# Kernel optimization log

Hardware: AMD Instinct MI355X
Metric: run time of the kernel (lower is better)

Reference implementation:

```python
import jax, jax.numpy as jnp
import numpy as np

N = 50000          # nodes
E = 1_600_000      # directed edges (before self loops)
G = 128            # graphs in batch
IN_F = 64
C1, H = 32, 4      # gat1: out_channels=32, heads=4 -> hidden 128
C2 = 64            # gat2: out_channels=64, heads=1, concat=False
OUT_F = 2
EPS = 1e-5
NEG_SLOPE = 0.2    # PyG GATv2Conv default


def setup_inputs() -> dict:
    key = jax.random.key(0)
    ks = jax.random.split(key, 24)
    s = 0.05
    inp = {
        'x': jax.random.normal(ks[0], (N, IN_F), jnp.float32),
        'edge_index': jax.random.randint(ks[1], (2, E), 0, N, dtype=jnp.int64),
        'batch': jnp.sort(jax.random.randint(ks[2], (N,), 0, G, dtype=jnp.int64)),
        # GATv2 layer 1 (in=64 -> 4 heads x 32)
        'W1l': jax.random.normal(ks[3], (IN_F, H * C1), jnp.float32) * s,
        'b1l': jnp.zeros((H * C1,), jnp.float32),
        'W1r': jax.random.normal(ks[4], (IN_F, H * C1), jnp.float32) * s,
        'b1r': jnp.zeros((H * C1,), jnp.float32),
        'att1': jax.random.normal(ks[5], (H, C1), jnp.float32) * s,
        'bias1': jnp.zeros((H * C1,), jnp.float32),
        # GATv2 layer 2 (in=128 -> 1 head x 64, no concat)
        'W2l': jax.random.normal(ks[6], (H * C1, C2), jnp.float32) * s,
        'b2l': jnp.zeros((C2,), jnp.float32),
        'W2r': jax.random.normal(ks[7], (H * C1, C2), jnp.float32) * s,
        'b2r': jnp.zeros((C2,), jnp.float32),
        'att2': jax.random.normal(ks[8], (1, C2), jnp.float32) * s,
        'bias2': jnp.zeros((C2,), jnp.float32),
        # batchnorms (batch-statistics normalization)
        'bn1_g': jnp.ones((H * C1,), jnp.float32),
        'bn1_b': jnp.zeros((H * C1,), jnp.float32),
        'bn2_g': jnp.ones((C2,), jnp.float32),
        'bn2_b': jnp.zeros((C2,), jnp.float32),
        # final linear: CL2_F*3 -> out_f
        'lin_w': jax.random.normal(ks[9], (3 * C2, OUT_F), jnp.float32) * s,
        'lin_b': jnp.zeros((OUT_F,), jnp.float32),
    }
    return inp


def _gatv2(x, Wl, bl, Wr, br, att, bias, src, dst, heads, ch, concat, n_nodes):
    # x: [N, F_in]; src/dst: [E'] (self loops already appended)
    xl = (x @ Wl + bl).reshape(n_nodes, heads, ch)  # source transform
    xr = (x @ Wr + br).reshape(n_nodes, heads, ch)  # target transform
    m = jax.nn.leaky_relu(xl[src] + xr[dst], NEG_SLOPE)      # [E', H, C]
    logits = jnp.einsum('ehc,hc->eh', m, att)                # [E', H]
    # segment softmax over destination nodes (every node has a self loop)
    mx = jax.ops.segment_max(logits, dst, num_segments=n_nodes)
    a = jnp.exp(logits - mx[dst])
    denom = jax.ops.segment_sum(a, dst, num_segments=n_nodes)
    alpha = a / denom[dst]                                   # [E', H]
    out = jax.ops.segment_sum(xl[src] * alpha[..., None], dst,
                              num_segments=n_nodes)          # [N, H, C]
    if concat:
        out = out.reshape(n_nodes, heads * ch)
    else:
        out = out.mean(axis=1)
    return out + bias


def _bn(h, gamma, beta):
    mu = h.mean(axis=0)
    var = h.var(axis=0)
    return (h - mu) * jax.lax.rsqrt(var + EPS) * gamma + beta


def reference(x, edge_index, batch, W1l, b1l, W1r, b1r, att1, bias1,
              W2l, b2l, W2r, b2r, att2, bias2,
              bn1_g, bn1_b, bn2_g, bn2_b, lin_w, lin_b):
    n = x.shape[0]
    loops = jnp.arange(n, dtype=edge_index.dtype)
    src = jnp.concatenate([edge_index[0], loops])  # PyG add_self_loops=True
    dst = jnp.concatenate([edge_index[1], loops])

    h = jax.nn.relu(_gatv2(x, W1l, b1l, W1r, b1r, att1, bias1,
                           src, dst, H, C1, True, n))
    h = _bn(h, bn1_g, bn1_b)      # dropout is identity (eval)
    h = jax.nn.relu(_gatv2(h, W2l, b2l, W2r, b2r, att2, bias2,
                           src, dst, 1, C2, False, n))
    h = _bn(h, bn2_g, bn2_b)

    x0 = jax.ops.segment_sum(h, batch, num_segments=G)                  # add pool
    cnt = jax.ops.segment_sum(jnp.ones((n, 1), h.dtype), batch, num_segments=G)
    x1 = x0 / jnp.maximum(cnt, 1.0)                                     # mean pool
    x2 = jax.ops.segment_max(h, batch, num_segments=G)                  # max pool
    feat = jnp.concatenate([x0, x1, x2], axis=-1)                       # [G, 3*C2]
    return feat @ lin_w + lin_b
```

## Files before the change

kernel.cpp:

```cpp
#include <hip/hip_runtime.h>
#include <hip/hip_fp16.h>
#include <math.h>

#define BSHIFT 7
#define CHUNK  8192
#define CAP    6144

__device__ inline __half2 habs2_(__half2 x){
  union { __half2 h; unsigned u; } c; c.h = x; c.u &= 0x7FFF7FFFu; return c.h;
}
__device__ inline __half2 lrelu2_(__half2 x, __half2 c06, __half2 c04){
  return __hfma2(c04, habs2_(x), __hmul2(c06, x));
}

__global__ __launch_bounds__(256) void k_bucket(const int* __restrict__ ei, int E, int N, int NB,
    int* __restrict__ bfill, unsigned* __restrict__ ebuf){
  extern __shared__ int hist[];
  int base = blockIdx.x*CHUNK;
  int EL = E + N;
  int end = min(base + CHUNK, EL);
  for (int i = threadIdx.x; i < NB; i += 256) hist[i] = 0;
  __syncthreads();
  for (int e = base + threadIdx.x; e < end; e += 256){
    int d = (e < E) ? ei[E + e] : (e - E);
    atomicAdd(&hist[d >> BSHIFT], 1);
  }
  __syncthreads();
  for (int b = threadIdx.x; b < NB; b += 256){
    int c = hist[b];
    hist[b] = (c > 0) ? (b*CAP + atomicAdd(&bfill[b], c)) : 0;
  }
  __syncthreads();
  for (int e = base + threadIdx.x; e < end; e += 256){
    int s, d;
    if (e < E){ s = ei[e]; d = ei[E + e]; } else { s = d = e - E; }
    int pos = atomicAdd(&hist[d >> BSHIFT], 1);
    ebuf[pos] = (unsigned)s | ((unsigned)d << 16);
  }
}

__global__ __launch_bounds__(1024) void k_fine(const unsigned* __restrict__ ebuf,
    const int* __restrict__ bfill, int N, int NB,
    int* __restrict__ rstart, int* __restrict__ rend, int* __restrict__ esrc){
  __shared__ int cnt[128];
  __shared__ int sc[128];
  __shared__ int base[128];
  int b = blockIdx.x;
  int n0 = b << BSHIFT;
  int nn = min(128, N - n0);
  int e0 = b*CAP;
  int e1 = e0 + bfill[b];
  if (threadIdx.x < 128) cnt[threadIdx.x] = 0;
  __syncthreads();
  for (int e = e0 + threadIdx.x; e < e1; e += 1024)
    atomicAdd(&cnt[(ebuf[e] >> 16) & 127], 1);
  __syncthreads();
  if (threadIdx.x < 128) sc[threadIdx.x] = cnt[threadIdx.x];
  __syncthreads();
  for (int off = 1; off < 128; off <<= 1){
    int v = 0;
    if (threadIdx.x < 128 && (int)threadIdx.x >= off) v = sc[threadIdx.x - off];
    __syncthreads();
    if (threadIdx.x < 128) sc[threadIdx.x] += v;
    __syncthreads();
  }
  if (threadIdx.x < 128){
    int bs = e0 + sc[threadIdx.x] - cnt[threadIdx.x];
    base[threadIdx.x] = bs;
    if ((int)threadIdx.x < nn){
      rstart[n0 + threadIdx.x] = bs;
      rend[n0 + threadIdx.x]   = bs + cnt[threadIdx.x];
    }
    cnt[threadIdx.x] = 0;
  }
  __syncthreads();
  for (int e = e0 + threadIdx.x; e < e1; e += 1024){
    unsigned pk = ebuf[e];
    int local = (int)(pk >> 16) & 127;
    int pos = base[local] + atomicAdd(&cnt[local], 1);
    esrc[pos] = (int)(pk & 0xffffu);
  }
}

template<int K, int COLS, bool BN, bool INHALF>
__global__ __launch_bounds__(256) void k_gemm(const void* __restrict__ Xv,
    const float* __restrict__ Wl, const float* __restrict__ bl,
    const float* __restrict__ Wr, const float* __restrict__ br,
    __half* __restrict__ outl, __half* __restrict__ outr, int N,
    const float* __restrict__ mu, const float* __restrict__ rstd,
    const float* __restrict__ gam, const float* __restrict__ bet){
  constexpr int HALF = COLS/2;
  constexpr int JG   = COLS/4;
  constexpr int NGRP = 256/JG;
  constexpr int NPG  = 32/NGRP;
  __shared__ float xs[32][K];
  const int tid = threadIdx.x;
  const int n0 = blockIdx.x*32;
  if constexpr (INHALF){
    const __half2* X2 = (const __half2*)Xv;
    for (int t = tid; t < 32*(K/2); t += 256){
      int r = t / (K/2), c2 = t % (K/2), c = c2*2;
      int node = n0 + r;
      float2 v = (node < N) ? __half22float2(X2[(size_t)node*(K/2) + c2]) : make_float2(0.f,0.f);
      if (BN){
        v.x = (v.x - mu[c  ]) * rstd[c  ] * gam[c  ] + bet[c  ];
        v.y = (v.y - mu[c+1]) * rstd[c+1] * gam[c+1] + bet[c+1];
      }
      xs[r][c] = v.x; xs[r][c+1] = v.y;
    }
  } else {
    const float* X = (const float*)Xv;
    for (int t = tid; t < 32*K; t += 256){
      int r = t / K, c = t % K;
      int node = n0 + r;
      xs[r][c] = (node < N) ? X[(size_t)node*K + c] : 0.f;
    }
  }
  __syncthreads();
  const int jg = tid % JG;
  const int ng = tid / JG;
  const int q  = jg*4;
  const bool isL = (q < HALF);
  const float* W = isL ? Wl : Wr;
  const int jj   = isL ? q : q - HALF;
  const float* bb = isL ? bl : br;
  __half* OUT    = isL ? outl : outr;
  const float4 bias4 = *(const float4*)(bb + jj);
  float acc[NPG][4];
  #pragma unroll
  for (int n = 0; n < NPG; ++n){ acc[n][0]=acc[n][1]=acc[n][2]=acc[n][3]=0.f; }
  for (int k = 0; k < K; k += 4){
    const float4 w0 = *(const float4*)(W + (size_t)(k+0)*HALF + jj);
    const float4 w1 = *(const float4*)(W + (size_t)(k+1)*HALF + jj);
    const float4 w2 = *(const float4*)(W + (size_t)(k+2)*HALF + jj);
    const float4 w3 = *(const float4*)(W + (size_t)(k+3)*HALF + jj);
    #pragma unroll
    for (int n = 0; n < NPG; ++n){
      const float4 xv = *(const float4*)(&xs[ng*NPG + n][k]);
      acc[n][0] = fmaf(xv.w,w3.x, fmaf(xv.z,w2.x, fmaf(xv.y,w1.x, fmaf(xv.x,w0.x, acc[n][0]))));
      acc[n][1] = fmaf(xv.w,w3.y, fmaf(xv.z,w2.y, fmaf(xv.y,w1.y, fmaf(xv.x,w0.y, acc[n][1]))));
      acc[n][2] = fmaf(xv.w,w3.z, fmaf(xv.z,w2.z, fmaf(xv.y,w1.z, fmaf(xv.x,w0.z, acc[n][2]))));
      acc[n][3] = fmaf(xv.w,w3.w, fmaf(xv.z,w2.w, fmaf(xv.y,w1.w, fmaf(xv.x,w0.w, acc[n][3]))));
    }
  }
  #pragma unroll
  for (int n = 0; n < NPG; ++n){
    int node = n0 + ng*NPG + n;
    if (node < N){
      union { __half2 h[2]; uint2 u; } cv;
      cv.h[0] = __floats2half2_rn(acc[n][0]+bias4.x, acc[n][1]+bias4.y);
      cv.h[1] = __floats2half2_rn(acc[n][2]+bias4.z, acc[n][3]+bias4.w);
      *(uint2*)(OUT + (size_t)node*HALF + jj) = cv.u;
    }
  }
}

__global__ __launch_bounds__(256) void k_gat1(const __half* __restrict__ xl, const __half* __restrict__ xr,
    const int* __restrict__ rstart, const int* __restrict__ rend,
    const int* __restrict__ esrc,
    const float* __restrict__ att, const float* __restrict__ bias,
    __half* __restrict__ h1, int N){
  int wv = (blockIdx.x*256 + threadIdx.x) >> 6;
  int lane = threadIdx.x & 63;
  int g = lane >> 4;
  int t = lane & 15;
  int node = wv*4 + g;
  bool live = node < N;
  int nd = live ? node : 0;
  int c0 = t*8;
  const __half2 c06 = __float2half2_rn(0.6f);
  const __half2 c04 = __float2half2_rn(0.4f);
  union { uint4 u; __half2 h[4]; } xru;
  xru.u = *(const uint4*)(xr + (size_t)nd*128 + c0);
  float4 a0 = *(const float4*)(att + c0);
  float4 a1 = *(const float4*)(att + c0 + 4);
  __half2 av2[4] = { __floats2half2_rn(a0.x,a0.y), __floats2half2_rn(a0.z,a0.w),
                     __floats2half2_rn(a1.x,a1.y), __floats2half2_rn(a1.z,a1.w) };
  int r0 = live ? rstart[nd] : 0;
  int r1 = live ? rend[nd]   : 0;
  int d  = r1 - r0;
  d = max(d, __shfl_xor(d, 16));
  d = max(d, __shfl_xor(d, 32));
  float s = 0.f;
  __half2 acc2[4];
  #pragma unroll
  for (int k = 0; k < 4; ++k) acc2[k] = __float2half2_rn(0.f);
  #pragma unroll 2
  for (int i = 0; i < d; ++i){
    int e = r0 + i;
    bool valid = e < r1;
    int j = esrc[valid ? e : r0];
    union { uint4 u; __half2 h[4]; } v;
    v.u = *(const uint4*)(xl + (size_t)j*128 + c0);
    __half2 p2 = __float2half2_rn(0.f);
    #pragma unroll
    for (int k = 0; k < 4; ++k){
      __half2 m2 = __hadd2(v.h[k], xru.h[k]);
      p2 = __hfma2(lrelu2_(m2, c06, c04), av2[k], p2);
    }
    float p = __low2float(p2) + __high2float(p2);
    p += __shfl_xor(p, 1);
    p += __shfl_xor(p, 2);
    float w = valid ? __expf(p) : 0.f;
    s += w;
    __half2 w2 = __float2half2_rn(w);
    #pragma unroll
    for (int k = 0; k < 4; ++k) acc2[k] = __hfma2(w2, v.h[k], acc2[k]);
  }
  if (live){
    float inv = 1.f/s;
    float4 b0 = *(const float4*)(bias + c0);
    float4 b1 = *(const float4*)(bias + c0 + 4);
    float bv[8] = {b0.x,b0.y,b0.z,b0.w,b1.x,b1.y,b1.z,b1.w};
    union { __half2 h[4]; uint4 u; } o;
    #pragma unroll
    for (int k = 0; k < 4; ++k){
      float2 af = __half22float2(acc2[k]);
      float f0 = fmaxf(af.x*inv + bv[2*k],   0.f);
      float f1 = fmaxf(af.y*inv + bv[2*k+1], 0.f);
      o.h[k] = __floats2half2_rn(f0, f1);
    }
    *(uint4*)(h1 + (size_t)nd*128 + c0) = o.u;
  }
}

__global__ __launch_bounds__(256) void k_gat2(const __half* __restrict__ xl, const __half* __restrict__ xr,
    const int* __restrict__ rstart, const int* __restrict__ rend,
    const int* __restrict__ esrc,
    const float* __restrict__ att, const float* __restrict__ bias,
    __half* __restrict__ h2, int N){
  int wv = (blockIdx.x*256 + threadIdx.x) >> 6;
  int lane = threadIdx.x & 63;
  int g = lane >> 3;
  int t = lane & 7;
  int node = wv*8 + g;
  bool live = node < N;
  int nd = live ? node : 0;
  int c0 = t*8;
  const __half2 c06 = __float2half2_rn(0.6f);
  const __half2 c04 = __float2half2_rn(0.4f);
  union { uint4 u; __half2 h[4]; } xru;
  xru.u = *(const uint4*)(xr + (size_t)nd*64 + c0);
  float4 a0 = *(const float4*)(att + c0);
  float4 a1 = *(const float4*)(att + c0 + 4);
  __half2 av2[4] = { __floats2half2_rn(a0.x,a0.y), __floats2half2_rn(a0.z,a0.w),
                     __floats2half2_rn(a1.x,a1.y), __floats2half2_rn(a1.z,a1.w) };
  int r0 = live ? rstart[nd] : 0;
  int r1 = live ? rend[nd]   : 0;
  int d  = r1 - r0;
  d = max(d, __shfl_xor(d, 8));
  d = max(d, __shfl_xor(d, 16));
  d = max(d, __shfl_xor(d, 32));
  float s = 0.f;
  __half2 acc2[4];
  #pragma unroll
  for (int k = 0; k < 4; ++k) acc2[k] = __float2half2_rn(0.f);
  #pragma unroll 2
  for (int i = 0; i < d; ++i){
    int e = r0 + i;
    bool valid = e < r1;
    int j = esrc[valid ? e : r0];
    union { uint4 u; __half2 h[4]; } v;
    v.u = *(const uint4*)(xl + (size_t)j*64 + c0);
    __half2 p2 = __float2half2_rn(0.f);
    #pragma unroll
    for (int k = 0; k < 4; ++k){
      __half2 m2 = __hadd2(v.h[k], xru.h[k]);
      p2 = __hfma2(lrelu2_(m2, c06, c04), av2[k], p2);
    }
    float p = __low2float(p2) + __high2float(p2);
    p += __shfl_xor(p, 1);
    p += __shfl_xor(p, 2);
    p += __shfl_xor(p, 4);
    float w = valid ? __expf(p) : 0.f;
    s += w;
    __half2 w2 = __float2half2_rn(w);
    #pragma unroll
    for (int k = 0; k < 4; ++k) acc2[k] = __hfma2(w2, v.h[k], acc2[k]);
  }
  if (live){
    float inv = 1.f/s;
    float4 b0 = *(const float4*)(bias + c0);
    float4 b1 = *(const float4*)(bias + c0 + 4);
    float bv[8] = {b0.x,b0.y,b0.z,b0.w,b1.x,b1.y,b1.z,b1.w};
    union { __half2 h[4]; uint4 u; } o;
    #pragma unroll
    for (int k = 0; k < 4; ++k){
      float2 af = __half22float2(acc2[k]);
      float f0 = fmaxf(af.x*inv + bv[2*k],   0.f);
      float f1 = fmaxf(af.y*inv + bv[2*k+1], 0.f);
      o.h[k] = __floats2half2_rn(f0, f1);
    }
    *(uint4*)(h2 + (size_t)nd*64 + c0) = o.u;
  }
}

template<int C>
__global__ __launch_bounds__(256) void k_bnstats(const __half* __restrict__ h, int N,
    float* __restrict__ sum, float* __restrict__ sq){
  constexpr int RPB = 256/C;
  int c = threadIdx.x % C;
  int sub = threadIdx.x / C;
  float s = 0.f, q = 0.f;
  for (int r = blockIdx.x*RPB + sub; r < N; r += gridDim.x*RPB){
    float v = __half2float(h[(size_t)r*C + c]);
    s += v; q += v*v;
  }
  __shared__ float ls[256], lq[256];
  ls[threadIdx.x] = s; lq[threadIdx.x] = q;
  __syncthreads();
  if (threadIdx.x < C){
    float S = ls[c], Q = lq[c];
    #pragma unroll
    for (int u = 1; u < RPB; ++u){ S += ls[u*C + c]; Q += lq[u*C + c]; }
    atomicAdd(&sum[c], S);
    atomicAdd(&sq[c], Q);
  }
}

__global__ void k_bnfinal(const float* __restrict__ sum, const float* __restrict__ sq, int N, int C,
                          float* __restrict__ mu, float* __restrict__ rstd){
  int c = threadIdx.x;
  if (c < C){
    float m = sum[c] / (float)N;
    float v = sq[c] / (float)N - m*m;
    mu[c] = m;
    rstd[c] = rsqrtf(v + 1e-5f);
  }
}

__global__ __launch_bounds__(256) void k_pool(const __half* __restrict__ h2, const int* __restrict__ batch, int N,
    const float* __restrict__ mu, const float* __restrict__ rstd,
    const float* __restrict__ g, const float* __restrict__ b,
    float* __restrict__ feat){
  int gr = blockIdx.x;
  int lo = 0, hi = N;
  while (lo < hi){ int mid = (lo+hi)>>1; if (batch[mid] < gr) lo = mid+1; else hi = mid; }
  int r0 = lo;
  lo = r0; hi = N;
  while (lo < hi){ int mid = (lo+hi)>>1; if (batch[mid] < gr+1) lo = mid+1; else hi = mid; }
  int r1 = lo;
  int c = threadIdx.x & 63;
  int sub = threadIdx.x >> 6;
  float aff_s = rstd[c]*g[c];
  float aff_b = b[c] - mu[c]*aff_s;
  float s = 0.f, mx = -INFINITY;
  for (int r = r0 + sub; r < r1; r += 4){
    float v = __half2float(h2[(size_t)r*64 + c])*aff_s + aff_b;
    s += v; mx = fmaxf(mx, v);
  }
  __shared__ float ls[256], lm[256];
  ls[threadIdx.x] = s; lm[threadIdx.x] = mx;
  __syncthreads();
  if (threadIdx.x < 64){
    float S = ls[c] + ls[64+c] + ls[128+c] + ls[192+c];
    float M = fmaxf(fmaxf(lm[c], lm[64+c]), fmaxf(lm[128+c], lm[192+c]));
    float cnt = (float)max(r1 - r0, 1);
    feat[gr*192 + c]       = S;
    feat[gr*192 + 64 + c]  = S/cnt;
    feat[gr*192 + 128 + c] = M;
  }
}

__global__ void k_head(const float* __restrict__ feat, const float* __restrict__ lw,
                       const float* __restrict__ lb, float* __restrict__ out, int G){
  int t = threadIdx.x;
  if (t >= G*2) return;
  int g = t >> 1, o = t & 1;
  float acc = lb[o];
  #pragma unroll 4
  for (int c = 0; c < 192; ++c) acc += feat[g*192 + c] * lw[c*2 + o];
  out[g*2 + o] = acc;
}

extern "C" void kernel_launch(void* const* d_in, const int* in_sizes, int n_in,
                              void* d_out, int out_size, void* d_ws, size_t ws_size,
                              hipStream_t stream) {
  const float* x    = (const float*)d_in[0];
  const int*   ei   = (const int*)d_in[1];
  const int*   batch= (const int*)d_in[2];
  const float* W1l  = (const float*)d_in[3];
  const float* b1l  = (const float*)d_in[4];
  const float* W1r  = (const float*)d_in[5];
  const float* b1r  = (const float*)d_in[6];
  const float* att1 = (const float*)d_in[7];
  const float* bias1= (const float*)d_in[8];
  const float* W2l  = (const float*)d_in[9];
  const float* b2l  = (const float*)d_in[10];
  const float* W2r  = (const float*)d_in[11];
  const float* b2r  = (const float*)d_in[12];
  const float* att2 = (const float*)d_in[13];
  const float* bias2= (const float*)d_in[14];
  const float* g1   = (const float*)d_in[15];
  const float* be1  = (const float*)d_in[16];
  const float* g2   = (const float*)d_in[17];
  const float* be2  = (const float*)d_in[18];
  const float* lw   = (const float*)d_in[19];
  const float* lb   = (const float*)d_in[20];

  const int N  = in_sizes[0] / 64;
  const int E  = in_sizes[1] / 2;
  const int EL = E + N;
  const int G  = 128;
  const int NB = (N + 127) >> BSHIFT;

  char* p = (char*)d_ws;
  auto carve = [&](size_t bytes)->char*{ char* r = p; p += (bytes + 255) & ~(size_t)255; return r; };
  int* zero   = (int*)carve((size_t)(NB + 384)*4);
  int* bfill  = zero;
  float* stats = (float*)(zero + NB);
  float* bn1_sum = stats;
  float* bn1_sq  = stats + 128;
  float* bn2_sum = stats + 256;
  float* bn2_sq  = stats + 320;
  int* rstart = (int*)carve((size_t)N*4);
  int* rend   = (int*)carve((size_t)N*4);
  unsigned* ebuf = (unsigned*)carve((size_t)NB*CAP*4);
  int* esrc   = (int*)carve((size_t)NB*CAP*4);
  __half* xl1 = (__half*)carve((size_t)N*128*2);
  __half* xr1 = (__half*)carve((size_t)N*128*2);
  __half* h1  = (__half*)carve((size_t)N*128*2);
  __half* xl2 = xl1;
  __half* xr2 = xl1 + (size_t)N*64;
  __half* h2  = xr1;
  float* bn1_mu  = (float*)carve((size_t)(128+128+64+64)*4);
  float* bn1_rstd= bn1_mu + 128;
  float* bn2_mu  = bn1_mu + 256;
  float* bn2_rstd= bn1_mu + 320;
  float* feat    = (float*)carve((size_t)G*192*4);

  hipMemsetAsync(zero, 0, (size_t)(NB + 384)*4, stream);

  const int bb = (EL + CHUNK - 1)/CHUNK;
  k_bucket<<<bb, 256, (size_t)NB*4, stream>>>(ei, E, N, NB, bfill, ebuf);
  k_fine  <<<NB, 1024, 0, stream>>>(ebuf, bfill, N, NB, rstart, rend, esrc);

  const int gb = (N + 31)/32;
  const int nb1 = ((N + 3)/4*64 + 255)/256;
  const int nb2 = ((N + 7)/8*64 + 255)/256;
  k_gemm<64,256,false,false><<<gb, 256, 0, stream>>>(x, W1l, b1l, W1r, b1r, xl1, xr1, N,
                                                     nullptr, nullptr, nullptr, nullptr);
  k_gat1<<<nb1, 256, 0, stream>>>(xl1, xr1, rstart, rend, esrc, att1, bias1, h1, N);
  k_bnstats<128><<<256, 256, 0, stream>>>(h1, N, bn1_sum, bn1_sq);
  k_bnfinal<<<1, 128, 0, stream>>>(bn1_sum, bn1_sq, N, 128, bn1_mu, bn1_rstd);
  k_gemm<128,128,true,true><<<gb, 256, 0, stream>>>(h1, W2l, b2l, W2r, b2r, xl2, xr2, N,
                                                    bn1_mu, bn1_rstd, g1, be1);
  k_gat2<<<nb2, 256, 0, stream>>>(xl2, xr2, rstart, rend, esrc, att2, bias2, h2, N);
  k_bnstats<64><<<256, 256, 0, stream>>>(h2, N, bn2_sum, bn2_sq);
  k_bnfinal<<<1, 64, 0, stream>>>(bn2_sum, bn2_sq, N, 64, bn2_mu, bn2_rstd);
  k_pool<<<G, 256, 0, stream>>>(h2, batch, N, bn2_mu, bn2_rstd, g2, be2, feat);
  k_head<<<1, 256, 0, stream>>>(feat, lw, lb, (float*)d_out, G);
}
```

Measured before the change: 430.6 us.

## Fuse bucketing with layer-1 GEMM, batch edge gathers, fold head into pool

Merges the edge bucketing kernel and the first-layer feature GEMM into one launch, with block ranges dispatched by block index, so the two independent jobs share a grid and overlap. The GAT aggregation loops now gather eight neighbour indices and eight feature rows before computing, which raises memory-level parallelism on the irregular gathers. They also use byte-offset addressing with 32-bit shifts and occupancy hints in launch bounds. The final linear head moves into the pooling kernel, and the second GEMM becomes a specialized non-template kernel. Costs are more registers in the gather loops, which may hurt occupancy, and wasted loads on the tail of each batch of eight.

```diff
diff --git a/kernel.cpp b/kernel.cpp
--- a/kernel.cpp
+++ b/kernel.cpp
@@ -13,29 +13,81 @@
   return __hfma2(c04, habs2_(x), __hmul2(c06, x));
 }
 
-__global__ __launch_bounds__(256) void k_bucket(const int* __restrict__ ei, int E, int N, int NB,
-    int* __restrict__ bfill, unsigned* __restrict__ ebuf){
-  extern __shared__ int hist[];
-  int base = blockIdx.x*CHUNK;
-  int EL = E + N;
-  int end = min(base + CHUNK, EL);
-  for (int i = threadIdx.x; i < NB; i += 256) hist[i] = 0;
-  __syncthreads();
-  for (int e = base + threadIdx.x; e < end; e += 256){
-    int d = (e < E) ? ei[E + e] : (e - E);
-    atomicAdd(&hist[d >> BSHIFT], 1);
-  }
-  __syncthreads();
-  for (int b = threadIdx.x; b < NB; b += 256){
-    int c = hist[b];
-    hist[b] = (c > 0) ? (b*CAP + atomicAdd(&bfill[b], c)) : 0;
-  }
-  __syncthreads();
-  for (int e = base + threadIdx.x; e < end; e += 256){
-    int s, d;
-    if (e < E){ s = ei[e]; d = ei[E + e]; } else { s = d = e - E; }
-    int pos = atomicAdd(&hist[d >> BSHIFT], 1);
-    ebuf[pos] = (unsigned)s | ((unsigned)d << 16);
+__global__ __launch_bounds__(256) void k_pre(const int* __restrict__ ei, int E, int N, int NB,
+    int* __restrict__ bfill, unsigned* __restrict__ ebuf,
+    const float* __restrict__ X,
+    const float* __restrict__ Wl, const float* __restrict__ bl,
+    const float* __restrict__ Wr, const float* __restrict__ br,
+    __half* __restrict__ outl, __half* __restrict__ outr, int bb){
+  __shared__ float xs[32][64];
+  if ((int)blockIdx.x < bb){
+    int* hist = (int*)&xs[0][0];
+    int base = blockIdx.x*CHUNK;
+    int EL = E + N;
+    int end = min(base + CHUNK, EL);
+    for (int i = threadIdx.x; i < NB; i += 256) hist[i] = 0;
+    __syncthreads();
+    for (int e = base + threadIdx.x; e < end; e += 256){
+      int d = (e < E) ? ei[E + e] : (e - E);
+      atomicAdd(&hist[d >> BSHIFT], 1);
+    }
+    __syncthreads();
+    for (int b = threadIdx.x; b < NB; b += 256){
+      int c = hist[b];
+      hist[b] = (c > 0) ? (b*CAP + atomicAdd(&bfill[b], c)) : 0;
+    }
+    __syncthreads();
+    for (int e = base + threadIdx.x; e < end; e += 256){
+      int s, d;
+      if (e < E){ s = ei[e]; d = ei[E + e]; } else { s = d = e - E; }
+      int pos = atomicAdd(&hist[d >> BSHIFT], 1);
+      ebuf[pos] = (unsigned)s | ((unsigned)d << 16);
+    }
+  } else {
+    const int tid = threadIdx.x;
+    const int n0 = ((int)blockIdx.x - bb)*32;
+    for (int t = tid; t < 32*64; t += 256){
+      int r = t >> 6, c = t & 63;
+      int node = n0 + r;
+      xs[r][c] = (node < N) ? X[(size_t)node*64 + c] : 0.f;
+    }
+    __syncthreads();
+    const int jg = tid & 63;
+    const int ng = tid >> 6;
+    const int q  = jg*4;
+    const bool isL = (q < 128);
+    const float* W = isL ? Wl : Wr;
+    const int jj   = isL ? q : q - 128;
+    const float* bbp = isL ? bl : br;
+    __half* OUT    = isL ? outl : outr;
+    const float4 bias4 = *(const float4*)(bbp + jj);
+    float acc[8][4];
+    #pragma unroll
+    for (int n = 0; n < 8; ++n){ acc[n][0]=acc[n][1]=acc[n][2]=acc[n][3]=0.f; }
+    for (int k = 0; k < 64; k += 4){
+      const float4 w0 = *(const float4*)(W + (size_t)(k+0)*128 + jj);
+      const float4 w1 = *(const float4*)(W + (size_t)(k+1)*128 + jj);
+      const float4 w2 = *(const float4*)(W + (size_t)(k+2)*128 + jj);
+      const float4 w3 = *(const float4*)(W + (size_t)(k+3)*128 + jj);
+      #pragma unroll
+      for (int n = 0; n < 8; ++n){
+        const float4 xv = *(const float4*)(&xs[ng*8 + n][k]);
+        acc[n][0] = fmaf(xv.w,w3.x, fmaf(xv.z,w2.x, fmaf(xv.y,w1.x, fmaf(xv.x,w0.x, acc[n][0]))));
+        acc[n][1] = fmaf(xv.w,w3.y, fmaf(xv.z,w2.y, fmaf(xv.y,w1.y, fmaf(xv.x,w0.y, acc[n][1]))));
+        acc[n][2] = fmaf(xv.w,w3.z, fmaf(xv.z,w2.z, fmaf(xv.y,w1.z, fmaf(xv.x,w0.z, acc[n][2]))));
+        acc[n][3] = fmaf(xv.w,w3.w, fmaf(xv.z,w2.w, fmaf(xv.y,w1.w, fmaf(xv.x,w0.w, acc[n][3]))));
+      }
+    }
+    #pragma unroll
+    for (int n = 0; n < 8; ++n){
+      int node = n0 + ng*8 + n;
+      if (node < N){
+        union { __half2 h[2]; uint2 u; } cv;
+        cv.h[0] = __floats2half2_rn(acc[n][0]+bias4.x, acc[n][1]+bias4.y);
+        cv.h[1] = __floats2half2_rn(acc[n][2]+bias4.z, acc[n][3]+bias4.w);
+        *(uint2*)(OUT + (size_t)node*128 + jj) = cv.u;
+      }
+    }
   }
 }
 
@@ -82,61 +134,44 @@
   }
 }
 
-template<int K, int COLS, bool BN, bool INHALF>
-__global__ __launch_bounds__(256) void k_gemm(const void* __restrict__ Xv,
+__global__ __launch_bounds__(256) void k_gemm2(const __half2* __restrict__ X2,
     const float* __restrict__ Wl, const float* __restrict__ bl,
     const float* __restrict__ Wr, const float* __restrict__ br,
     __half* __restrict__ outl, __half* __restrict__ outr, int N,
     const float* __restrict__ mu, const float* __restrict__ rstd,
     const float* __restrict__ gam, const float* __restrict__ bet){
-  constexpr int HALF = COLS/2;
-  constexpr int JG   = COLS/4;
-  constexpr int NGRP = 256/JG;
-  constexpr int NPG  = 32/NGRP;
-  __shared__ float xs[32][K];
+  __shared__ float xs[32][128];
   const int tid = threadIdx.x;
   const int n0 = blockIdx.x*32;
-  if constexpr (INHALF){
-    const __half2* X2 = (const __half2*)Xv;
-    for (int t = tid; t < 32*(K/2); t += 256){
-      int r = t / (K/2), c2 = t % (K/2), c = c2*2;
-      int node = n0 + r;
-      float2 v = (node < N) ? __half22float2(X2[(size_t)node*(K/2) + c2]) : make_float2(0.f,0.f);
-      if (BN){
-        v.x = (v.x - mu[c  ]) * rstd[c  ] * gam[c  ] + bet[c  ];
-        v.y = (v.y - mu[c+1]) * rstd[c+1] * gam[c+1] + bet[c+1];
-      }
-      xs[r][c] = v.x; xs[r][c+1] = v.y;
-    }
-  } else {
-    const float* X = (const float*)Xv;
-    for (int t = tid; t < 32*K; t += 256){
-      int r = t / K, c = t % K;
-      int node = n0 + r;
-      xs[r][c] = (node < N) ? X[(size_t)node*K + c] : 0.f;
-    }
-  }
-  __syncthreads();
-  const int jg = tid % JG;
-  const int ng = tid / JG;
+  for (int t = tid; t < 32*64; t += 256){
+    int r = t >> 6, c2 = t & 63, c = c2*2;
+    int node = n0 + r;
+    float2 v = (node < N) ? __half22float2(X2[(size_t)node*64 + c2]) : make_float2(0.f,0.f);
+    v.x = (v.x - mu[c  ]) * rstd[c  ] * gam[c  ] + bet[c  ];
+    v.y = (v.y - mu[c+1]) * rstd[c+1] * gam[c+1] + bet[c+1];
+    xs[r][c] = v.x; xs[r][c+1] = v.y;
+  }
+  __syncthreads();
+  const int jg = tid & 31;
+  const int ng = tid >> 5;
   const int q  = jg*4;
-  const bool isL = (q < HALF);
+  const bool isL = (q < 64);
   const float* W = isL ? Wl : Wr;
-  const int jj   = isL ? q : q - HALF;
-  const float* bb = isL ? bl : br;
+  const int jj   = isL ? q : q - 64;
+  const float* bbp = isL ? bl : br;
   __half* OUT    = isL ? outl : outr;
-  const float4 bias4 = *(const float4*)(bb + jj);
-  float acc[NPG][4];
+  const float4 bias4 = *(const float4*)(bbp + jj);
+  float acc[4][4];
   #pragma unroll
-  for (int n = 0; n < NPG; ++n){ acc[n][0]=acc[n][1]=acc[n][2]=acc[n][3]=0.f; }
-  for (int k = 0; k < K; k += 4){
-    const float4 w0 = *(const float4*)(W + (size_t)(k+0)*HALF + jj);
-    const float4 w1 = *(const float4*)(W + (size_t)(k+1)*HALF + jj);
-    const float4 w2 = *(const float4*)(W + (size_t)(k+2)*HALF + jj);
-    const float4 w3 = *(const float4*)(W + (size_t)(k+3)*HALF + jj);
-    #pragma unroll
-    for (int n = 0; n < NPG; ++n){
-      const float4 xv = *(const float4*)(&xs[ng*NPG + n][k]);
+  for (int n = 0; n < 4; ++n){ acc[n][0]=acc[n][1]=acc[n][2]=acc[n][3]=0.f; }
+  for (int k = 0; k < 128; k += 4){
+    const float4 w0 = *(const float4*)(W + (size_t)(k+0)*64 + jj);
+    const float4 w1 = *(const float4*)(W + (size_t)(k+1)*64 + jj);
+    const float4 w2 = *(const float4*)(W + (size_t)(k+2)*64 + jj);
+    const float4 w3 = *(const float4*)(W + (size_t)(k+3)*64 + jj);
+    #pragma unroll
+    for (int n = 0; n < 4; ++n){
+      const float4 xv = *(const float4*)(&xs[ng*4 + n][k]);
       acc[n][0] = fmaf(xv.w,w3.x, fmaf(xv.z,w2.x, fmaf(xv.y,w1.x, fmaf(xv.x,w0.x, acc[n][0]))));
       acc[n][1] = fmaf(xv.w,w3.y, fmaf(xv.z,w2.y, fmaf(xv.y,w1.y, fmaf(xv.x,w0.y, acc[n][1]))));
       acc[n][2] = fmaf(xv.w,w3.z, fmaf(xv.z,w2.z, fmaf(xv.y,w1.z, fmaf(xv.x,w0.z, acc[n][2]))));
@@ -144,18 +179,18 @@
     }
   }
   #pragma unroll
-  for (int n = 0; n < NPG; ++n){
-    int node = n0 + ng*NPG + n;
+  for (int n = 0; n < 4; ++n){
+    int node = n0 + ng*4 + n;
     if (node < N){
       union { __half2 h[2]; uint2 u; } cv;
       cv.h[0] = __floats2half2_rn(acc[n][0]+bias4.x, acc[n][1]+bias4.y);
       cv.h[1] = __floats2half2_rn(acc[n][2]+bias4.z, acc[n][3]+bias4.w);
-      *(uint2*)(OUT + (size_t)node*HALF + jj) = cv.u;
-    }
-  }
-}
-
-__global__ __launch_bounds__(256) void k_gat1(const __half* __restrict__ xl, const __half* __restrict__ xr,
+      *(uint2*)(OUT + (size_t)node*64 + jj) = cv.u;
+    }
+  }
+}
+
+__global__ __launch_bounds__(256, 6) void k_gat1(const __half* __restrict__ xl, const __half* __restrict__ xr,
     const int* __restrict__ rstart, const int* __restrict__ rend,
     const int* __restrict__ esrc,
     const float* __restrict__ att, const float* __restrict__ bias,
@@ -181,31 +216,41 @@
   int d  = r1 - r0;
   d = max(d, __shfl_xor(d, 16));
   d = max(d, __shfl_xor(d, 32));
+  const char* xb = (const char*)xl;
+  const unsigned cb = (unsigned)(c0*2);
   float s = 0.f;
   __half2 acc2[4];
   #pragma unroll
   for (int k = 0; k < 4; ++k) acc2[k] = __float2half2_rn(0.f);
-  #pragma unroll 2
-  for (int i = 0; i < d; ++i){
-    int e = r0 + i;
-    bool valid = e < r1;
-    int j = esrc[valid ? e : r0];
-    union { uint4 u; __half2 h[4]; } v;
-    v.u = *(const uint4*)(xl + (size_t)j*128 + c0);
-    __half2 p2 = __float2half2_rn(0.f);
-    #pragma unroll
-    for (int k = 0; k < 4; ++k){
-      __half2 m2 = __hadd2(v.h[k], xru.h[k]);
-      p2 = __hfma2(lrelu2_(m2, c06, c04), av2[k], p2);
-    }
-    float p = __low2float(p2) + __high2float(p2);
-    p += __shfl_xor(p, 1);
-    p += __shfl_xor(p, 2);
-    float w = valid ? __expf(p) : 0.f;
-    s += w;
-    __half2 w2 = __float2half2_rn(w);
-    #pragma unroll
-    for (int k = 0; k < 4; ++k) acc2[k] = __hfma2(w2, v.h[k], acc2[k]);
+  for (int i = 0; i < d; i += 8){
+    unsigned jj[8];
+    #pragma unroll
+    for (int q = 0; q < 8; ++q){
+      int e = r0 + i + q;
+      jj[q] = (unsigned)esrc[e < r1 ? e : r0];
+    }
+    union { uint4 u; __half2 h[4]; } v[8];
+    #pragma unroll
+    for (int q = 0; q < 8; ++q)
+      v[q].u = *(const uint4*)(xb + ((jj[q] << 8) + cb));
+    #pragma unroll
+    for (int q = 0; q < 8; ++q){
+      bool valid = (r0 + i + q) < r1;
+      __half2 p2 = __float2half2_rn(0.f);
+      #pragma unroll
+      for (int k = 0; k < 4; ++k){
+        __half2 m2 = __hadd2(v[q].h[k], xru.h[k]);
+        p2 = __hfma2(lrelu2_(m2, c06, c04), av2[k], p2);
+      }
+      float p = __low2float(p2) + __high2float(p2);
+      p += __shfl_xor(p, 1);
+      p += __shfl_xor(p, 2);
+      float w = valid ? __expf(p) : 0.f;
+      s += w;
+      __half2 w2 = __float2half2_rn(w);
+      #pragma unroll
+      for (int k = 0; k < 4; ++k) acc2[k] = __hfma2(w2, v[q].h[k], acc2[k]);
+    }
   }
   if (live){
     float inv = 1.f/s;
@@ -224,7 +269,7 @@
   }
 }
 
-__global__ __launch_bounds__(256) void k_gat2(const __half* __restrict__ xl, const __half* __restrict__ xr,
+__global__ __launch_bounds__(256, 6) void k_gat2(const __half* __restrict__ xl, const __half* __restrict__ xr,
     const int* __restrict__ rstart, const int* __restrict__ rend,
     const int* __restrict__ esrc,
     const float* __restrict__ att, const float* __restrict__ bias,
@@ -251,32 +296,42 @@
   d = max(d, __shfl_xor(d, 8));
   d = max(d, __shfl_xor(d, 16));
   d = max(d, __shfl_xor(d, 32));
+  const char* xb = (const char*)xl;
+  const unsigned cb = (unsigned)(c0*2);
   float s = 0.f;
   __half2 acc2[4];
   #pragma unroll
   for (int k = 0; k < 4; ++k) acc2[k] = __float2half2_rn(0.f);
-  #pragma unroll 2
-  for (int i = 0; i < d; ++i){
-    int e = r0 + i;
-    bool valid = e < r1;
-    int j = esrc[valid ? e : r0];
-    union { uint4 u; __half2 h[4]; } v;
-    v.u = *(const uint4*)(xl + (size_t)j*64 + c0);
-    __half2 p2 = __float2half2_rn(0.f);
-    #pragma unroll
-    for (int k = 0; k < 4; ++k){
-      __half2 m2 = __hadd2(v.h[k], xru.h[k]);
-      p2 = __hfma2(lrelu2_(m2, c06, c04), av2[k], p2);
-    }
-    float p = __low2float(p2) + __high2float(p2);
-    p += __shfl_xor(p, 1);
-    p += __shfl_xor(p, 2);
-    p += __shfl_xor(p, 4);
-    float w = valid ? __expf(p) : 0.f;
-    s += w;
-    __half2 w2 = __float2half2_rn(w);
-    #pragma unroll
-    for (int k = 0; k < 4; ++k) acc2[k] = __hfma2(w2, v.h[k], acc2[k]);
+  for (int i = 0; i < d; i += 8){
+    unsigned jj[8];
+    #pragma unroll
+    for (int q = 0; q < 8; ++q){
+      int e = r0 + i + q;
+      jj[q] = (unsigned)esrc[e < r1 ? e : r0];
+    }
+    union { uint4 u; __half2 h[4]; } v[8];
+    #pragma unroll
+    for (int q = 0; q < 8; ++q)
+      v[q].u = *(const uint4*)(xb + ((jj[q] << 7) + cb));
+    #pragma unroll
+    for (int q = 0; q < 8; ++q){
+      bool valid = (r0 + i + q) < r1;
+      __half2 p2 = __float2half2_rn(0.f);
+      #pragma unroll
+      for (int k = 0; k < 4; ++k){
+        __half2 m2 = __hadd2(v[q].h[k], xru.h[k]);
+        p2 = __hfma2(lrelu2_(m2, c06, c04), av2[k], p2);
+      }
+      float p = __low2float(p2) + __high2float(p2);
+      p += __shfl_xor(p, 1);
+      p += __shfl_xor(p, 2);
+      p += __shfl_xor(p, 4);
+      float w = valid ? __expf(p) : 0.f;
+      s += w;
+      __half2 w2 = __float2half2_rn(w);
+      #pragma unroll
+      for (int k = 0; k < 4; ++k) acc2[k] = __hfma2(w2, v[q].h[k], acc2[k]);
+    }
   }
   if (live){
     float inv = 1.f/s;
@@ -332,7 +387,8 @@
 __global__ __launch_bounds__(256) void k_pool(const __half* __restrict__ h2, const int* __restrict__ batch, int N,
     const float* __restrict__ mu, const float* __restrict__ rstd,
     const float* __restrict__ g, const float* __restrict__ b,
-    float* __restrict__ feat){
+    const float* __restrict__ lw, const float* __restrict__ lb,
+    float* __restrict__ out){
   int gr = blockIdx.x;
   int lo = 0, hi = N;
   while (lo < hi){ int mid = (lo+hi)>>1; if (batch[mid] < gr) lo = mid+1; else hi = mid; }
@@ -349,28 +405,24 @@
     float v = __half2float(h2[(size_t)r*64 + c])*aff_s + aff_b;
     s += v; mx = fmaxf(mx, v);
   }
-  __shared__ float ls[256], lm[256];
+  __shared__ float ls[256], lm[256], ft[192];
   ls[threadIdx.x] = s; lm[threadIdx.x] = mx;
   __syncthreads();
   if (threadIdx.x < 64){
     float S = ls[c] + ls[64+c] + ls[128+c] + ls[192+c];
     float M = fmaxf(fmaxf(lm[c], lm[64+c]), fmaxf(lm[128+c], lm[192+c]));
     float cnt = (float)max(r1 - r0, 1);
-    feat[gr*192 + c]       = S;
-    feat[gr*192 + 64 + c]  = S/cnt;
-    feat[gr*192 + 128 + c] = M;
-  }
-}
-
-__global__ void k_head(const float* __restrict__ feat, const float* __restrict__ lw,
-                       const float* __restrict__ lb, float* __restrict__ out, int G){
-  int t = threadIdx.x;
-  if (t >= G*2) return;
-  int g = t >> 1, o = t & 1;
-  float acc = lb[o];
-  #pragma unroll 4
-  for (int c = 0; c < 192; ++c) acc += feat[g*192 + c] * lw[c*2 + o];
-  out[g*2 + o] = acc;
+    ft[c]       = S;
+    ft[64 + c]  = S/cnt;
+    ft[128 + c] = M;
+  }
+  __syncthreads();
+  if (threadIdx.x < 2){
+    float acc = lb[threadIdx.x];
+    #pragma unroll 4
+    for (int k = 0; k < 192; ++k) acc += ft[k] * lw[k*2 + threadIdx.x];
+    out[gr*2 + threadIdx.x] = acc;
+  }
 }
 
 extern "C" void kernel_launch(void* const* d_in, const int* in_sizes, int n_in,
@@ -427,27 +479,24 @@
   float* bn1_rstd= bn1_mu + 128;
   float* bn2_mu  = bn1_mu + 256;
   float* bn2_rstd= bn1_mu + 320;
-  float* feat    = (float*)carve((size_t)G*192*4);
 
   hipMemsetAsync(zero, 0, (size_t)(NB + 384)*4, stream);
 
   const int bb = (EL + CHUNK - 1)/CHUNK;
-  k_bucket<<<bb, 256, (size_t)NB*4, stream>>>(ei, E, N, NB, bfill, ebuf);
-  k_fine  <<<NB, 1024, 0, stream>>>(ebuf, bfill, N, NB, rstart, rend, esrc);
-
   const int gb = (N + 31)/32;
+  k_pre<<<bb + gb, 256, 0, stream>>>(ei, E, N, NB, bfill, ebuf,
+                                     x, W1l, b1l, W1r, b1r, xl1, xr1, bb);
+  k_fine<<<NB, 1024, 0, stream>>>(ebuf, bfill, N, NB, rstart, rend, esrc);
+
   const int nb1 = ((N + 3)/4*64 + 255)/256;
   const int nb2 = ((N + 7)/8*64 + 255)/256;
-  k_gemm<64,256,false,false><<<gb, 256, 0, stream>>>(x, W1l, b1l, W1r, b1r, xl1, xr1, N,
-                                                     nullptr, nullptr, nullptr, nullptr);
   k_gat1<<<nb1, 256, 0, stream>>>(xl1, xr1, rstart, rend, esrc, att1, bias1, h1, N);
   k_bnstats<128><<<256, 256, 0, stream>>>(h1, N, bn1_sum, bn1_sq);
   k_bnfinal<<<1, 128, 0, stream>>>(bn1_sum, bn1_sq, N, 128, bn1_mu, bn1_rstd);
-  k_gemm<128,128,true,true><<<gb, 256, 0, stream>>>(h1, W2l, b2l, W2r, b2r, xl2, xr2, N,
-                                                    bn1_mu, bn1_rstd, g1, be1);
+  k_gemm2<<<gb, 256, 0, stream>>>((const __half2*)h1, W2l, b2l, W2r, b2r, xl2, xr2, N,
+                                  bn1_mu, bn1_rstd, g1, be1);
   k_gat2<<<nb2, 256, 0, stream>>>(xl2, xr2, rstart, rend, esrc, att2, bias2, h2, N);
   k_bnstats<64><<<256, 256, 0, stream>>>(h2, N, bn2_sum, bn2_sq);
   k_bnfinal<<<1, 64, 0, stream>>>(bn2_sum, bn2_sq, N, 64, bn2_mu, bn2_rstd);
-  k_pool<<<G, 256, 0, stream>>>(h2, batch, N, bn2_mu, bn2_rstd, g2, be2, feat);
-  k_head<<<1, 256, 0, stream>>>(feat, lw, lb, (float*)d_out, G);
-}
+  k_pool<<<G, 256, 0, stream>>>(h2, batch, N, bn2_mu, bn2_rstd, g2, be2, lw, lb, (float*)d_out);
+}
```

New measurement: 381.0 us. 11.5% less time.
